# Kernel tuning notes

Hardware: AMD Instinct MI355X
Metric: run time of the kernel (lower is better)

Reference implementation:

```python
import jax, jax.numpy as jnp
import numpy as np

D_MODEL = 768
NUM_HEADS = 12
HEAD_DIM = D_MODEL // NUM_HEADS
SEQ = 4096
BATCH = 1


def setup_inputs() -> dict:
    key = jax.random.key(0)
    ks = jax.random.split(key, 6)
    scale = 1.0 / np.sqrt(D_MODEL)
    x = jax.random.normal(ks[0], (BATCH, SEQ, D_MODEL), dtype=jnp.float32)
    mask = jnp.tril(jnp.ones((SEQ, SEQ), dtype=bool))[None, None]  # [1,1,S,S] causal
    Wq = jax.random.normal(ks[1], (D_MODEL, D_MODEL), dtype=jnp.float32) * scale
    Wk = jax.random.normal(ks[2], (D_MODEL, D_MODEL), dtype=jnp.float32) * scale
    Wv = jax.random.normal(ks[3], (D_MODEL, D_MODEL), dtype=jnp.float32) * scale
    Wo = jax.random.normal(ks[4], (D_MODEL, D_MODEL), dtype=jnp.float32) * scale
    bo = jax.random.normal(ks[5], (D_MODEL,), dtype=jnp.float32) * 0.01
    return {"x": x, "mask": mask, "Wq": Wq, "Wk": Wk, "Wv": Wv, "Wo": Wo, "bo": bo}


def _rope_tables(seq_len, head_dim, dtype):
    # inv_freq over even dims; emb = cat(freqs, freqs) but only the first half
    # participates in the well-defined rotation (x1/x2 have head_dim//2 channels)
    inv_freq = 1.0 / (10000.0 ** (jnp.arange(0, head_dim, 2, dtype=dtype) / head_dim))
    t = jnp.arange(seq_len, dtype=dtype)
    freqs = t[:, None] * inv_freq[None, :]  # [S, head_dim//2]
    return jnp.cos(freqs), jnp.sin(freqs)


def _apply_rotary(xh, cos, sin):
    # xh: [B,H,S,hd]; cos/sin: [S, hd//2]
    x1 = xh[..., ::2]
    x2 = xh[..., 1::2]
    # faithful to source: concatenated (not interleaved) rotated halves
    return jnp.concatenate([x1 * cos - x2 * sin, x1 * sin + x2 * cos], axis=-1)


def reference(x, mask, Wq, Wk, Wv, Wo, bo):
    B, S, D = x.shape
    H, hd = NUM_HEADS, HEAD_DIM
    def split_heads(y):
        return y.reshape(B, S, H, hd).transpose(0, 2, 1, 3)  # [B,H,S,hd]
    q = split_heads(x @ Wq.T)
    k = split_heads(x @ Wk.T)
    v = split_heads(x @ Wv.T)
    cos, sin = _rope_tables(S, hd, x.dtype)
    q = _apply_rotary(q, cos, sin)
    k = _apply_rotary(k, cos, sin)
    scores = jnp.einsum('bhqd,bhkd->bhqk', q, k) / jnp.sqrt(jnp.asarray(hd, x.dtype))
    scores = jnp.where(mask, scores, jnp.asarray(-1e9, x.dtype))
    attn = jax.nn.softmax(scores, axis=-1)  # dropout is identity in eval
    out = jnp.einsum('bhqk,bhkd->bhqd', attn, v)
    out = out.transpose(0, 2, 1, 3).reshape(B, S, D)
    return out @ Wo.T + bo
```

## Files before the change

kernel.cpp:

```cpp
#include <hip/hip_runtime.h>
#include <hip/hip_bf16.h>
#include <math.h>

#define SEQ 4096
#define DM  768
#define NH  12
#define HD  64
#define PER ((size_t)NH * SEQ * HD)
#define XN  ((size_t)SEQ * DM)
#define WN  ((size_t)DM * DM)

typedef __attribute__((ext_vector_type(8))) short bf16x8;
typedef __attribute__((ext_vector_type(4))) short s16x4;
typedef __attribute__((ext_vector_type(4))) float f32x4;

#define MFMA(a, b, c) __builtin_amdgcn_mfma_f32_16x16x32_bf16((a), (b), (c), 0, 0, 0)

#if __has_builtin(__builtin_amdgcn_exp2f)
#define EXP2(x) __builtin_amdgcn_exp2f(x)
#else
#define EXP2(x) exp2f(x)
#endif

#define SWZ(row, blk) (((row) << 6) + ((((blk) ^ ((row) & 7))) << 3))

__device__ __forceinline__ unsigned short f2b(float f) {
    unsigned int u = __float_as_uint(f);
    u += 0x7FFFu + ((u >> 16) & 1u);
    return (unsigned short)(u >> 16);
}

__global__ __launch_bounds__(256) void prep_kernel(
    const float* __restrict__ x,  const float* __restrict__ wq,
    const float* __restrict__ wk, const float* __restrict__ wv,
    const float* __restrict__ wo,
    unsigned short* __restrict__ dstbase, float2* __restrict__ rope)
{
    const float* srcs[5] = {x, wq, wk, wv, wo};
    const size_t n4s[5]  = {XN / 4, WN / 4, WN / 4, WN / 4, WN / 4};
    unsigned short* d = dstbase;
    for (int rg = 0; rg < 5; ++rg) {
        const float4* s4 = (const float4*)srcs[rg];
        s16x4* d4 = (s16x4*)d;
        for (size_t i = (size_t)blockIdx.x * 256 + threadIdx.x; i < n4s[rg];
             i += (size_t)gridDim.x * 256) {
            const float4 v = s4[i];
            s16x4 p;
            p.x = (short)f2b(v.x); p.y = (short)f2b(v.y);
            p.z = (short)f2b(v.z); p.w = (short)f2b(v.w);
            d4[i] = p;
        }
        d += n4s[rg] * 4;
    }
    for (int g = blockIdx.x * 256 + threadIdx.x; g < 131072; g += gridDim.x * 256) {
        const int row = g >> 5, fi = g & 31;
        const float invf = expf(-(float)fi * 0.28782313662425576f);
        float sn, cs;
        sincosf((float)row * invf, &sn, &cs);
        rope[row * 32 + fi] = make_float2(cs, sn);
    }
}

__global__ __launch_bounds__(256) void qkv_mfma(
    const float* __restrict__ x,  const unsigned short* __restrict__ xb,
    const float* __restrict__ Wq, const float* __restrict__ Wk, const float* __restrict__ Wv,
    const unsigned short* __restrict__ Wqb, const unsigned short* __restrict__ Wkb,
    const unsigned short* __restrict__ Wvb,
    const float2* __restrict__ rope,
    unsigned short* __restrict__ Qo, unsigned short* __restrict__ Ko,
    unsigned short* __restrict__ Vo, int fast)
{
    __shared__ __align__(16) unsigned short Xs[2][4096];
    __shared__ __align__(16) unsigned short Ws[2][3][4096];
    __shared__ unsigned short VL[64 * 66];

    const int t    = threadIdx.x;
    const int w    = t >> 6;
    const int lane = t & 63;
    const int quad = lane >> 4;
    const int l16  = lane & 15;

    const int gid = blockIdx.y * 64 + blockIdx.x;
    const int Wl  = (gid & 7) * 96 + (gid >> 3);
    const int h   = Wl % 12;
    const int s0  = (Wl / 12) * 64;
    const int n0  = h * 64;

    const unsigned short* Wbs[3] = {Wqb, Wkb, Wvb};
    const float*          Wfs[3] = {Wq, Wk, Wv};

    const int rowb = 32 * (w >> 1);
    const int colb = 32 * (w & 1);

    f32x4 acc[3][2][2];
    #pragma unroll
    for (int rg = 0; rg < 3; ++rg)
        #pragma unroll
        for (int mi = 0; mi < 2; ++mi)
            #pragma unroll
            for (int ni = 0; ni < 2; ++ni) acc[rg][mi][ni] = (f32x4){0,0,0,0};

    const int prow = t >> 3, pblk = t & 7;

    bf16x8 xr0, xr1, wr0[3], wr1[3];
    if (fast) {
        xr0 = *(const bf16x8*)&xb[(size_t)(s0 + prow) * DM + pblk * 8];
        xr1 = *(const bf16x8*)&xb[(size_t)(s0 + prow + 32) * DM + pblk * 8];
        #pragma unroll
        for (int rg = 0; rg < 3; ++rg) {
            wr0[rg] = *(const bf16x8*)&Wbs[rg][(size_t)(n0 + prow) * DM + pblk * 8];
            wr1[rg] = *(const bf16x8*)&Wbs[rg][(size_t)(n0 + prow + 32) * DM + pblk * 8];
        }
        *(bf16x8*)&Xs[0][SWZ(prow, pblk)]      = xr0;
        *(bf16x8*)&Xs[0][SWZ(prow + 32, pblk)] = xr1;
        #pragma unroll
        for (int rg = 0; rg < 3; ++rg) {
            *(bf16x8*)&Ws[0][rg][SWZ(prow, pblk)]      = wr0[rg];
            *(bf16x8*)&Ws[0][rg][SWZ(prow + 32, pblk)] = wr1[rg];
        }
    } else {
        for (int e = t; e < 1024; e += 256) {
            const int row = e >> 4, c4 = e & 15;
            const int off = SWZ(row, c4 >> 1) + (c4 & 1) * 4;
            const float4 xv = *(const float4*)&x[(size_t)(s0 + row) * DM + c4 * 4];
            s16x4 px; px.x = (short)f2b(xv.x); px.y = (short)f2b(xv.y);
            px.z = (short)f2b(xv.z); px.w = (short)f2b(xv.w);
            *(s16x4*)&Xs[0][off] = px;
            #pragma unroll
            for (int rg = 0; rg < 3; ++rg) {
                const float4 wv = *(const float4*)&Wfs[rg][(size_t)(n0 + row) * DM + c4 * 4];
                s16x4 pw; pw.x = (short)f2b(wv.x); pw.y = (short)f2b(wv.y);
                pw.z = (short)f2b(wv.z); pw.w = (short)f2b(wv.w);
                *(s16x4*)&Ws[0][rg][off] = pw;
            }
        }
    }
    __syncthreads();

    for (int kt = 0; kt < 12; ++kt) {
        const unsigned short* Xb = Xs[kt & 1];
        if (fast && kt < 11) {
            const int k0 = (kt + 1) * 64;
            xr0 = *(const bf16x8*)&xb[(size_t)(s0 + prow) * DM + k0 + pblk * 8];
            xr1 = *(const bf16x8*)&xb[(size_t)(s0 + prow + 32) * DM + k0 + pblk * 8];
            #pragma unroll
            for (int rg = 0; rg < 3; ++rg) {
                wr0[rg] = *(const bf16x8*)&Wbs[rg][(size_t)(n0 + prow) * DM + k0 + pblk * 8];
                wr1[rg] = *(const bf16x8*)&Wbs[rg][(size_t)(n0 + prow + 32) * DM + k0 + pblk * 8];
            }
        }
        bf16x8 a[2][2];
        #pragma unroll
        for (int mi = 0; mi < 2; ++mi)
            #pragma unroll
            for (int hh = 0; hh < 2; ++hh)
                a[mi][hh] = *(const bf16x8*)&Xb[SWZ(rowb + 16 * mi + l16, 4 * hh + quad)];
        #pragma unroll
        for (int rg = 0; rg < 3; ++rg) {
            const unsigned short* Wbt = Ws[kt & 1][rg];
            #pragma unroll
            for (int ni = 0; ni < 2; ++ni) {
                const bf16x8 b0 = *(const bf16x8*)&Wbt[SWZ(colb + 16 * ni + l16, quad)];
                const bf16x8 b1 = *(const bf16x8*)&Wbt[SWZ(colb + 16 * ni + l16, 4 + quad)];
                #pragma unroll
                for (int mi = 0; mi < 2; ++mi) {
                    acc[rg][mi][ni] = MFMA(a[mi][0], b0, acc[rg][mi][ni]);
                    acc[rg][mi][ni] = MFMA(a[mi][1], b1, acc[rg][mi][ni]);
                }
            }
        }
        if (kt < 11) {
            const int nb = (kt + 1) & 1;
            if (fast) {
                *(bf16x8*)&Xs[nb][SWZ(prow, pblk)]      = xr0;
                *(bf16x8*)&Xs[nb][SWZ(prow + 32, pblk)] = xr1;
                #pragma unroll
                for (int rg = 0; rg < 3; ++rg) {
                    *(bf16x8*)&Ws[nb][rg][SWZ(prow, pblk)]      = wr0[rg];
                    *(bf16x8*)&Ws[nb][rg][SWZ(prow + 32, pblk)] = wr1[rg];
                }
            } else {
                const int k0 = (kt + 1) * 64;
                for (int e = t; e < 1024; e += 256) {
                    const int row = e >> 4, c4 = e & 15;
                    const int off = SWZ(row, c4 >> 1) + (c4 & 1) * 4;
                    const float4 xv = *(const float4*)&x[(size_t)(s0 + row) * DM + k0 + c4 * 4];
                    s16x4 px; px.x = (short)f2b(xv.x); px.y = (short)f2b(xv.y);
                    px.z = (short)f2b(xv.z); px.w = (short)f2b(xv.w);
                    *(s16x4*)&Xs[nb][off] = px;
                    #pragma unroll
                    for (int rg = 0; rg < 3; ++rg) {
                        const float4 wv = *(const float4*)&Wfs[rg][(size_t)(n0 + row) * DM + k0 + c4 * 4];
                        s16x4 pw; pw.x = (short)f2b(wv.x); pw.y = (short)f2b(wv.y);
                        pw.z = (short)f2b(wv.z); pw.w = (short)f2b(wv.w);
                        *(s16x4*)&Ws[nb][rg][off] = pw;
                    }
                }
            }
        }
        __syncthreads();
    }

    const size_t headoff = (size_t)h * SEQ * HD;
    #pragma unroll
    for (int rg = 0; rg < 2; ++rg) {
        unsigned short* dst = (rg == 0) ? Qo : Ko;
        const float qsc = (rg == 0) ? 0.18033688011112042f : 1.0f;
        #pragma unroll
        for (int mi = 0; mi < 2; ++mi)
            #pragma unroll
            for (int ni = 0; ni < 2; ++ni)
                #pragma unroll
                for (int r = 0; r < 4; ++r) {
                    const int srow = s0 + rowb + 16 * mi + quad * 4 + r;
                    const int d  = colb + 16 * ni + l16;
                    const int fi = d >> 1;
                    const float own = acc[rg][mi][ni][r] * qsc;
                    const float oth = __shfl_xor(own, 1);
                    float cs, sn;
                    if (fast) {
                        const float2 t2 = rope[srow * 32 + fi];
                        cs = t2.x; sn = t2.y;
                    } else {
                        const float invf = expf(-(float)fi * 0.28782313662425576f);
                        sincosf((float)srow * invf, &sn, &cs);
                    }
                    const float val = (d & 1) ? (oth * sn + own * cs)
                                              : (own * cs - oth * sn);
                    dst[headoff + (size_t)srow * HD + ((d & 1) ? 32 : 0) + fi] = f2b(val);
                }
    }
    #pragma unroll
    for (int mi = 0; mi < 2; ++mi)
        #pragma unroll
        for (int ni = 0; ni < 2; ++ni)
            #pragma unroll
            for (int r = 0; r < 4; ++r)
                VL[(colb + 16 * ni + l16) * 66 + rowb + 16 * mi + quad * 4 + r] =
                    f2b(acc[2][mi][ni][r]);
    __syncthreads();
    for (int e = t; e < 2048; e += 256) {
        const int d = e >> 5, sp = e & 31;
        const unsigned int v = (unsigned int)VL[d * 66 + 2 * sp] |
                               ((unsigned int)VL[d * 66 + 2 * sp + 1] << 16);
        *(unsigned int*)&Vo[headoff + (size_t)d * SEQ + s0 + 2 * sp] = v;
    }
}

__global__ __launch_bounds__(256, 2) void attn_mfma(
    const unsigned short* __restrict__ Q,
    const unsigned short* __restrict__ K,
    const unsigned short* __restrict__ V,
    unsigned short* __restrict__ O,
    float* __restrict__ Part)
{
    __shared__ __align__(16) unsigned char SM[53248];
    unsigned short* Kst = (unsigned short*)SM;
    unsigned short* Vt  = (unsigned short*)(SM + 16384);
    unsigned short* Ps  = (unsigned short*)(SM + 32768);
    float* ACC  = (float*)SM;
    float* ACC2 = (float*)(SM + 32768);
    float* Lx   = (float*)(SM + 51200);

    int h, xx;
    if (gridDim.x == 96) {
        const int gid = blockIdx.y * 96 + blockIdx.x;
        const int Wl  = (gid & 7) * 144 + (gid >> 3);
        h  = Wl / 96;
        xx = Wl - h * 96;
    } else {
        const int gid = blockIdx.y * 64 + blockIdx.x;
        const int Wl  = (gid & 7) * 96 + (gid >> 3);
        h  = Wl >> 6;
        xx = Wl & 63;
    }

    int i, kstart, nch, domask, partial, pslice;
    if (gridDim.x == 96) {
        if (xx < 64) {
            i = 63 - xx; kstart = 0;
            const int full = ((i * 64 + 63) >> 7) + 1;
            nch = full < 16 ? full : 16;
            domask  = (i <= 31);
            partial = (i >= 32); pslice = 0;
        } else {
            i = 127 - xx; kstart = 2048;
            nch = ((i * 64 + 63 - 2048) >> 7) + 1;
            domask = 1; partial = 1; pslice = 1;
        }
    } else {
        i = 63 - xx; kstart = 0;
        nch = ((i * 64 + 63) >> 7) + 1;
        domask = 1; partial = 0; pslice = 0;
    }
    const int q0 = i * 64;

    const int t    = threadIdx.x;
    const int w    = t >> 6;
    const int lane = t & 63;
    const int quad = lane >> 4;
    const int l16  = lane & 15;
    const size_t headoff = (size_t)h * SEQ * HD;

    for (int e = t; e < 512; e += 256) {
        const int row = e >> 3, bp = e & 7, blk = bp ^ (row & 7);
        *(bf16x8*)&Kst[row * 64 + bp * 8] =
            *(const bf16x8*)&Q[headoff + (size_t)(q0 + row) * HD + blk * 8];
    }
    __syncthreads();
    bf16x8 aQ[4][2];
    #pragma unroll
    for (int qt = 0; qt < 4; ++qt)
        #pragma unroll
        for (int hh = 0; hh < 2; ++hh)
            aQ[qt][hh] = *(const bf16x8*)&Kst[SWZ(16 * qt + l16, 4 * hh + quad)];
    __syncthreads();

    bf16x8 kreg[4], vreg[4];
    #pragma unroll
    for (int ii = 0; ii < 4; ++ii) {
        const int e = t + ii * 256, row = e >> 3, bp = e & 7, blk = bp ^ (row & 7);
        kreg[ii] = *(const bf16x8*)&K[headoff + (size_t)(kstart + row) * HD + blk * 8];
    }
    #pragma unroll
    for (int ii = 0; ii < 4; ++ii) {
        const int e = t + ii * 256, row = e >> 4, bp = e & 15, blk = bp ^ (row & 15);
        vreg[ii] = *(const bf16x8*)&V[headoff + (size_t)row * SEQ + kstart + blk * 8];
    }
    #pragma unroll
    for (int ii = 0; ii < 4; ++ii) {
        const int e = t + ii * 256, row = e >> 3, bp = e & 7;
        *(bf16x8*)&Kst[row * 64 + bp * 8] = kreg[ii];
    }
    #pragma unroll
    for (int ii = 0; ii < 4; ++ii) {
        const int e = t + ii * 256, row = e >> 4, bp = e & 15;
        *(bf16x8*)&Vt[row * 128 + bp * 8] = vreg[ii];
    }
    __syncthreads();

    bf16x8 ones;
    #pragma unroll
    for (int ii = 0; ii < 8; ++ii) ones[ii] = (short)0x3F80;

    f32x4 oT[4][4];
    #pragma unroll
    for (int dt = 0; dt < 4; ++dt)
        #pragma unroll
        for (int qt = 0; qt < 4; ++qt) oT[dt][qt] = (f32x4){0,0,0,0};
    f32x4 lT[4] = {{0,0,0,0},{0,0,0,0},{0,0,0,0},{0,0,0,0}};

    unsigned short* usp = Ps + w * 2560;

    for (int c = 0; c < nch; ++c) {
        const int k0 = kstart + c * 128;
        const int last = (c == nch - 1);

        bf16x8 bK[2][2];
        #pragma unroll
        for (int kt = 0; kt < 2; ++kt)
            #pragma unroll
            for (int hh = 0; hh < 2; ++hh)
                bK[kt][hh] = *(const bf16x8*)
                    &Kst[SWZ(32 * w + 16 * kt + l16, 4 * hh + quad)];
        bf16x8 aV[4];
        #pragma unroll
        for (int dt = 0; dt < 4; ++dt) {
            const int row = 16 * dt + l16;
            aV[dt] = *(const bf16x8*)&Vt[row * 128 + (((4 * w + quad) ^ (row & 15)) << 3)];
        }

        if (c + 1 < nch) {
            const int kn = k0 + 128;
            #pragma unroll
            for (int ii = 0; ii < 4; ++ii) {
                const int e = t + ii * 256, row = e >> 3, bp = e & 7, blk = bp ^ (row & 7);
                kreg[ii] = *(const bf16x8*)&K[headoff + (size_t)(kn + row) * HD + blk * 8];
            }
            #pragma unroll
            for (int ii = 0; ii < 4; ++ii) {
                const int e = t + ii * 256, row = e >> 4, bp = e & 15, blk = bp ^ (row & 15);
                vreg[ii] = *(const bf16x8*)&V[headoff + (size_t)row * SEQ + kn + blk * 8];
            }
        }

        #pragma unroll
        for (int qt = 0; qt < 4; ++qt) {
            f32x4 s0 = (f32x4){0,0,0,0}, s1 = (f32x4){0,0,0,0};
            #pragma unroll
            for (int hh = 0; hh < 2; ++hh) {
                s0 = MFMA(aQ[qt][hh], bK[0][hh], s0);
                s1 = MFMA(aQ[qt][hh], bK[1][hh], s1);
            }
            if (domask && last) {
                const int key0 = k0 + 32 * w + l16;
                #pragma unroll
                for (int r = 0; r < 4; ++r) {
                    const int qrow = q0 + 16 * qt + 4 * quad + r;
                    if (key0 > qrow)      s0[r] = -1e30f;
                    if (key0 + 16 > qrow) s1[r] = -1e30f;
                }
            }
            #pragma unroll
            for (int r = 0; r < 4; ++r) {
                const int row = (16 * qt + 4 * quad + r) * 40;
                usp[row + l16]      = f2b(EXP2(s0[r]));
                usp[row + 16 + l16] = f2b(EXP2(s1[r]));
            }
        }

        asm volatile("s_waitcnt lgkmcnt(0)" ::: "memory");

        __builtin_amdgcn_s_setprio(1);
        #pragma unroll
        for (int qt = 0; qt < 4; ++qt) {
            const bf16x8 bP = *(const bf16x8*)&usp[(16 * qt + l16) * 40 + quad * 8];
            lT[qt] = MFMA(ones, bP, lT[qt]);
            #pragma unroll
            for (int dt = 0; dt < 4; ++dt)
                oT[dt][qt] = MFMA(aV[dt], bP, oT[dt][qt]);
        }
        __builtin_amdgcn_s_setprio(0);

        __syncthreads();
        if (c + 1 < nch) {
            #pragma unroll
            for (int ii = 0; ii < 4; ++ii) {
                const int e = t + ii * 256, row = e >> 3, bp = e & 7;
                *(bf16x8*)&Kst[row * 64 + bp * 8] = kreg[ii];
            }
            #pragma unroll
            for (int ii = 0; ii < 4; ++ii) {
                const int e = t + ii * 256, row = e >> 4, bp = e & 15;
                *(bf16x8*)&Vt[row * 128 + bp * 8] = vreg[ii];
            }
        }
        __syncthreads();
    }

    if (w != 0 && quad == 0) {
        #pragma unroll
        for (int qt = 0; qt < 4; ++qt)
            Lx[w * 64 + 16 * qt + l16] = lT[qt][0];
    }
    if (w == 1) {
        #pragma unroll
        for (int dt = 0; dt < 4; ++dt)
            #pragma unroll
            for (int qt = 0; qt < 4; ++qt)
                *(f32x4*)&ACC[(16 * qt + l16) * 72 + 16 * dt + 4 * quad] = oT[dt][qt];
    }
    __syncthreads();
    if (w == 0) {
        #pragma unroll
        for (int dt = 0; dt < 4; ++dt)
            #pragma unroll
            for (int qt = 0; qt < 4; ++qt)
                oT[dt][qt] += *(const f32x4*)&ACC[(16 * qt + l16) * 72 + 16 * dt + 4 * quad];
    }
    if (w == 2) {
        #pragma unroll
        for (int dt = 0; dt < 4; ++dt)
            #pragma unroll
            for (int qt = 0; qt < 4; ++qt)
                *(f32x4*)&ACC2[(16 * qt + l16) * 72 + 16 * dt + 4 * quad] = oT[dt][qt];
    }
    __syncthreads();
    if (w == 0) {
        #pragma unroll
        for (int dt = 0; dt < 4; ++dt)
            #pragma unroll
            for (int qt = 0; qt < 4; ++qt)
                oT[dt][qt] += *(const f32x4*)&ACC2[(16 * qt + l16) * 72 + 16 * dt + 4 * quad];
    }
    if (w == 3) {
        #pragma unroll
        for (int dt = 0; dt < 4; ++dt)
            #pragma unroll
            for (int qt = 0; qt < 4; ++qt)
                *(f32x4*)&ACC[(16 * qt + l16) * 72 + 16 * dt + 4 * quad] = oT[dt][qt];
    }
    __syncthreads();
    if (w == 0) {
        float ls[4];
        #pragma unroll
        for (int qt = 0; qt < 4; ++qt) {
            #pragma unroll
            for (int dt = 0; dt < 4; ++dt)
                oT[dt][qt] += *(const f32x4*)&ACC[(16 * qt + l16) * 72 + 16 * dt + 4 * quad];
            ls[qt] = lT[qt][0] + Lx[64 + 16 * qt + l16] +
                     Lx[128 + 16 * qt + l16] + Lx[192 + 16 * qt + l16];
        }
        if (!partial) {
            #pragma unroll
            for (int qt = 0; qt < 4; ++qt) {
                const float inv = 1.0f / ls[qt];
                const size_t rowoff = (size_t)(q0 + 16 * qt + l16) * DM + h * HD;
                #pragma unroll
                for (int dt = 0; dt < 4; ++dt) {
                    ushort4 u;
                    u.x = f2b(oT[dt][qt][0] * inv);
                    u.y = f2b(oT[dt][qt][1] * inv);
                    u.z = f2b(oT[dt][qt][2] * inv);
                    u.w = f2b(oT[dt][qt][3] * inv);
                    *(ushort4*)&O[rowoff + 16 * dt + 4 * quad] = u;
                }
            }
        } else {
            float* P = Part + (size_t)(((i - 32) * 12 + h) * 2 + pslice) * 4160;
            #pragma unroll
            for (int dt = 0; dt < 4; ++dt)
                #pragma unroll
                for (int qt = 0; qt < 4; ++qt)
                    *(f32x4*)&P[(16 * qt + l16) * 64 + 16 * dt + 4 * quad] = oT[dt][qt];
            if (quad == 0) {
                #pragma unroll
                for (int qt = 0; qt < 4; ++qt)
                    P[4096 + 16 * qt + l16] = ls[qt];
            }
        }
    }
}

__global__ __launch_bounds__(256) void reduce_attn(
    const float* __restrict__ Part, unsigned short* __restrict__ O)
{
    const int b  = blockIdx.x;
    const int i  = 32 + b / 12, h = b % 12;
    const int q0 = i * 64;
    const float* P0 = Part + (size_t)(b * 2 + 0) * 4160;
    const float* P1 = Part + (size_t)(b * 2 + 1) * 4160;
    __shared__ float linv[64];
    const int t = threadIdx.x;
    if (t < 64) linv[t] = 1.0f / (P0[4096 + t] + P1[4096 + t]);
    __syncthreads();
    for (int idx = t; idx < 4096; idx += 256) {
        const int q = idx >> 6, d = idx & 63;
        const float v = (P0[q * 64 + d] + P1[q * 64 + d]) * linv[q];
        O[(size_t)(q0 + q) * DM + h * HD + d] = f2b(v);
    }
}

__global__ __launch_bounds__(256) void proj_mfma(
    const unsigned short* __restrict__ A,
    const float* __restrict__ Wo, const unsigned short* __restrict__ Wob,
    const float* __restrict__ bo,
    float* __restrict__ out, int fast)
{
    __shared__ __align__(16) unsigned short Xs[2][4096];
    __shared__ __align__(16) unsigned short Ws[2][4096];

    const int t    = threadIdx.x;
    const int w    = t >> 6;
    const int lane = t & 63;
    const int quad = lane >> 4;
    const int l16  = lane & 15;

    const int gid = blockIdx.y * 64 + blockIdx.x;
    const int Wl  = (gid & 7) * 96 + (gid >> 3);
    const int s0  = (Wl / 12) * 64;
    const int n0  = (Wl % 12) * 64;

    const int prow = t >> 3, pblk = t & 7;

    f32x4 acc[4] = {{0,0,0,0},{0,0,0,0},{0,0,0,0},{0,0,0,0}};

    bf16x8 ar0, ar1, wr0, wr1;
    ar0 = *(const bf16x8*)&A[(size_t)(s0 + prow) * DM + pblk * 8];
    ar1 = *(const bf16x8*)&A[(size_t)(s0 + prow + 32) * DM + pblk * 8];
    *(bf16x8*)&Xs[0][SWZ(prow, pblk)]      = ar0;
    *(bf16x8*)&Xs[0][SWZ(prow + 32, pblk)] = ar1;
    if (fast) {
        wr0 = *(const bf16x8*)&Wob[(size_t)(n0 + prow) * DM + pblk * 8];
        wr1 = *(const bf16x8*)&Wob[(size_t)(n0 + prow + 32) * DM + pblk * 8];
        *(bf16x8*)&Ws[0][SWZ(prow, pblk)]      = wr0;
        *(bf16x8*)&Ws[0][SWZ(prow + 32, pblk)] = wr1;
    } else {
        for (int e = t; e < 1024; e += 256) {
            const int row = e >> 4, c4 = e & 15;
            const float4 wv = *(const float4*)&Wo[(size_t)(n0 + row) * DM + c4 * 4];
            s16x4 pw; pw.x = (short)f2b(wv.x); pw.y = (short)f2b(wv.y);
            pw.z = (short)f2b(wv.z); pw.w = (short)f2b(wv.w);
            *(s16x4*)&Ws[0][SWZ(row, c4 >> 1) + (c4 & 1) * 4] = pw;
        }
    }
    __syncthreads();

    for (int kt = 0; kt < 12; ++kt) {
        const unsigned short* Xb  = Xs[kt & 1];
        const unsigned short* Wbt = Ws[kt & 1];
        if (kt < 11) {
            const int k0 = (kt + 1) * 64;
            ar0 = *(const bf16x8*)&A[(size_t)(s0 + prow) * DM + k0 + pblk * 8];
            ar1 = *(const bf16x8*)&A[(size_t)(s0 + prow + 32) * DM + k0 + pblk * 8];
            if (fast) {
                wr0 = *(const bf16x8*)&Wob[(size_t)(n0 + prow) * DM + k0 + pblk * 8];
                wr1 = *(const bf16x8*)&Wob[(size_t)(n0 + prow + 32) * DM + k0 + pblk * 8];
            }
        }
        const bf16x8 a0 = *(const bf16x8*)&Xb[SWZ(16 * w + l16, quad)];
        const bf16x8 a1 = *(const bf16x8*)&Xb[SWZ(16 * w + l16, 4 + quad)];
        #pragma unroll
        for (int nt = 0; nt < 4; ++nt) {
            const bf16x8 b0 = *(const bf16x8*)&Wbt[SWZ(16 * nt + l16, quad)];
            const bf16x8 b1 = *(const bf16x8*)&Wbt[SWZ(16 * nt + l16, 4 + quad)];
            acc[nt] = MFMA(a0, b0, acc[nt]);
            acc[nt] = MFMA(a1, b1, acc[nt]);
        }
        if (kt < 11) {
            const int nb = (kt + 1) & 1;
            *(bf16x8*)&Xs[nb][SWZ(prow, pblk)]      = ar0;
            *(bf16x8*)&Xs[nb][SWZ(prow + 32, pblk)] = ar1;
            if (fast) {
                *(bf16x8*)&Ws[nb][SWZ(prow, pblk)]      = wr0;
                *(bf16x8*)&Ws[nb][SWZ(prow + 32, pblk)] = wr1;
            } else {
                const int k0 = (kt + 1) * 64;
                for (int e = t; e < 1024; e += 256) {
                    const int row = e >> 4, c4 = e & 15;
                    const float4 wv = *(const float4*)&Wo[(size_t)(n0 + row) * DM + k0 + c4 * 4];
                    s16x4 pw; pw.x = (short)f2b(wv.x); pw.y = (short)f2b(wv.y);
                    pw.z = (short)f2b(wv.z); pw.w = (short)f2b(wv.w);
                    *(s16x4*)&Ws[nb][SWZ(row, c4 >> 1) + (c4 & 1) * 4] = pw;
                }
            }
        }
        __syncthreads();
    }

    #pragma unroll
    for (int nt = 0; nt < 4; ++nt)
        #pragma unroll
        for (int r = 0; r < 4; ++r) {
            const int srow = s0 + 16 * w + quad * 4 + r;
            const int n    = n0 + nt * 16 + l16;
            out[(size_t)srow * DM + n] = acc[nt][r] + bo[n];
        }
}

extern "C" void kernel_launch(void* const* d_in, const int* in_sizes, int n_in,
                              void* d_out, int out_size, void* d_ws, size_t ws_size,
                              hipStream_t stream) {
    const float* x  = (const float*)d_in[0];
    const float* Wq = (const float*)d_in[2];
    const float* Wk = (const float*)d_in[3];
    const float* Wv = (const float*)d_in[4];
    const float* Wo = (const float*)d_in[5];
    const float* bo = (const float*)d_in[6];
    float* out = (float*)d_out;

    unsigned short* U  = (unsigned short*)d_ws;
    unsigned short* Qw = U;
    unsigned short* Kw = U + PER;
    unsigned short* Vw = U + 2 * PER;
    unsigned short* Ow = U + 3 * PER;
    unsigned short* xb  = U + 4 * PER;
    unsigned short* Wqb = xb + XN;
    unsigned short* Wkb = Wqb + WN;
    unsigned short* Wvb = Wkb + WN;
    unsigned short* Wob = Wvb + WN;
    float2* rope = (float2*)(Wob + WN);
    float*  part = (float*)(rope + 4096 * 32);
    const size_t need  = (char*)part - (char*)d_ws;
    const size_t need2 = need + (size_t)384 * 2 * 4160 * 4;
    const int fast  = (ws_size >= need)  ? 1 : 0;
    const int split = (ws_size >= need2) ? 1 : 0;

    if (fast)
        prep_kernel<<<1024, 256, 0, stream>>>(x, Wq, Wk, Wv, Wo, xb, rope);
    qkv_mfma<<<dim3(64, 12), 256, 0, stream>>>(
        x, xb, Wq, Wk, Wv, Wqb, Wkb, Wvb, rope, Qw, Kw, Vw, fast);
    if (split) {
        attn_mfma<<<dim3(96, NH), 256, 0, stream>>>(Qw, Kw, Vw, Ow, part);
        reduce_attn<<<dim3(384), 256, 0, stream>>>(part, Ow);
    } else {
        attn_mfma<<<dim3(64, NH), 256, 0, stream>>>(Qw, Kw, Vw, Ow, part);
    }
    proj_mfma<<<dim3(SEQ / 64, DM / 64), 256, 0, stream>>>(Ow, Wo, Wob, bo, out, fast);
}
```

Baseline: 232.9 us.

## Split causal attention KV range into up to four 1024-key slices per query tile

Replaces the two-way KV split for the upper half of query tiles with a split-K scheme that cuts each query tile's causal key range into 1024-key slices (1 to 4 slices depending on position). The grid grows from 1152 to 1920 blocks, which balances work across CUs and shortens the longest block. The reduce kernel now sums a variable number of partials for tiles 16..63. In exchange there are more partial-result writes and reads, extra workspace, and more redundant Q loads.

```diff
diff --git a/kernel.cpp b/kernel.cpp
--- a/kernel.cpp
+++ b/kernel.cpp
@@ -262,36 +262,31 @@
     float* ACC2 = (float*)(SM + 32768);
     float* Lx   = (float*)(SM + 51200);
 
-    int h, xx;
-    if (gridDim.x == 96) {
-        const int gid = blockIdx.y * 96 + blockIdx.x;
-        const int Wl  = (gid & 7) * 144 + (gid >> 3);
-        h  = Wl / 96;
-        xx = Wl - h * 96;
+    int h, i, kstart, nch, domask, partial, sidx;
+    if (gridDim.x == 1920) {
+        const int gid = blockIdx.x;
+        const int Wl  = (gid & 7) * 240 + (gid >> 3);
+        h = Wl / 160;
+        const int r = Wl % 160;
+        if (r < 64)       { i = 63 - (r >> 2); sidx = r & 3; }
+        else if (r < 112) { const int q = r - 64; const int d3 = q / 3;
+                            i = 47 - d3; sidx = q - 3 * d3; }
+        else if (r < 144) { const int q = r - 112; i = 31 - (q >> 1); sidx = q & 1; }
+        else              { i = 15 - (r - 144); sidx = 0; }
+        const int nsl  = (i >> 4) + 1;
+        kstart = sidx << 10;
+        const int kend = (sidx == nsl - 1) ? (i + 1) * 64 : ((sidx + 1) << 10);
+        nch     = (kend - kstart + 127) >> 7;
+        domask  = (sidx == nsl - 1);
+        partial = (nsl > 1);
     } else {
         const int gid = blockIdx.y * 64 + blockIdx.x;
         const int Wl  = (gid & 7) * 96 + (gid >> 3);
-        h  = Wl >> 6;
-        xx = Wl & 63;
-    }
-
-    int i, kstart, nch, domask, partial, pslice;
-    if (gridDim.x == 96) {
-        if (xx < 64) {
-            i = 63 - xx; kstart = 0;
-            const int full = ((i * 64 + 63) >> 7) + 1;
-            nch = full < 16 ? full : 16;
-            domask  = (i <= 31);
-            partial = (i >= 32); pslice = 0;
-        } else {
-            i = 127 - xx; kstart = 2048;
-            nch = ((i * 64 + 63 - 2048) >> 7) + 1;
-            domask = 1; partial = 1; pslice = 1;
-        }
-    } else {
+        h = Wl >> 6;
+        const int xx = Wl & 63;
         i = 63 - xx; kstart = 0;
         nch = ((i * 64 + 63) >> 7) + 1;
-        domask = 1; partial = 0; pslice = 0;
+        domask = 1; partial = 0; sidx = 0;
     }
     const int q0 = i * 64;
 
@@ -507,7 +502,7 @@
                 }
             }
         } else {
-            float* P = Part + (size_t)(((i - 32) * 12 + h) * 2 + pslice) * 4160;
+            float* P = Part + (size_t)((i * 12 + h) * 4 + sidx) * 4160;
             #pragma unroll
             for (int dt = 0; dt < 4; ++dt)
                 #pragma unroll
@@ -525,19 +520,24 @@
 __global__ __launch_bounds__(256) void reduce_attn(
     const float* __restrict__ Part, unsigned short* __restrict__ O)
 {
-    const int b  = blockIdx.x;
-    const int i  = 32 + b / 12, h = b % 12;
-    const int q0 = i * 64;
-    const float* P0 = Part + (size_t)(b * 2 + 0) * 4160;
-    const float* P1 = Part + (size_t)(b * 2 + 1) * 4160;
+    const int b   = blockIdx.x;
+    const int i   = 16 + b / 12, h = b % 12;
+    const int q0  = i * 64;
+    const int nsl = (i >> 4) + 1;
+    const float* P0 = Part + (size_t)((i * 12 + h) * 4) * 4160;
     __shared__ float linv[64];
     const int t = threadIdx.x;
-    if (t < 64) linv[t] = 1.0f / (P0[4096 + t] + P1[4096 + t]);
+    if (t < 64) {
+        float sum = 0.f;
+        for (int s = 0; s < nsl; ++s) sum += P0[(size_t)s * 4160 + 4096 + t];
+        linv[t] = 1.0f / sum;
+    }
     __syncthreads();
     for (int idx = t; idx < 4096; idx += 256) {
         const int q = idx >> 6, d = idx & 63;
-        const float v = (P0[q * 64 + d] + P1[q * 64 + d]) * linv[q];
-        O[(size_t)(q0 + q) * DM + h * HD + d] = f2b(v);
+        float v = 0.f;
+        for (int s = 0; s < nsl; ++s) v += P0[(size_t)s * 4160 + idx];
+        O[(size_t)(q0 + q) * DM + h * HD + d] = f2b(v * linv[q]);
     }
 }
 
@@ -662,7 +662,7 @@
     float2* rope = (float2*)(Wob + WN);
     float*  part = (float*)(rope + 4096 * 32);
     const size_t need  = (char*)part - (char*)d_ws;
-    const size_t need2 = need + (size_t)384 * 2 * 4160 * 4;
+    const size_t need2 = need + (size_t)3072 * 4160 * 4;
     const int fast  = (ws_size >= need)  ? 1 : 0;
     const int split = (ws_size >= need2) ? 1 : 0;
 
@@ -671,10 +671,10 @@
     qkv_mfma<<<dim3(64, 12), 256, 0, stream>>>(
         x, xb, Wq, Wk, Wv, Wqb, Wkb, Wvb, rope, Qw, Kw, Vw, fast);
     if (split) {
-        attn_mfma<<<dim3(96, NH), 256, 0, stream>>>(Qw, Kw, Vw, Ow, part);
-        reduce_attn<<<dim3(384), 256, 0, stream>>>(part, Ow);
+        attn_mfma<<<dim3(1920, 1), 256, 0, stream>>>(Qw, Kw, Vw, Ow, part);
+        reduce_attn<<<dim3(576), 256, 0, stream>>>(part, Ow);
     } else {
-        attn_mfma<<<dim3(64, NH), 256, 0, stream>>>(Qw, Kw, Vw, Ow, part);
+        attn_mfma<<<dim3(64, 12), 256, 0, stream>>>(Qw, Kw, Vw, Ow, part);
     }
     proj_mfma<<<dim3(SEQ / 64, DM / 64), 256, 0, stream>>>(Ow, Wo, Wob, bo, out, fast);
 }
```

New measurement: 253.1 us. +8.6%, slower.

## Load K and V MFMA fragments directly from global memory, dropping LDS staging

Applied to the files above, without the earlier changes.

The attention kernel no longer stages K and V chunks through shared memory with two block-wide barriers per chunk. Each wave loads its own K and V MFMA operand fragments straight from global memory into registers, prefetching the next K chunk during the PV phase. This cuts LDS traffic and synchronization and shrinks shared memory, which may allow more resident blocks. The cost is global loads with less coalescing, partly strided V reads across SEQ, and V loads that are no longer prefetched, so their latency may be exposed.

```diff
diff --git a/kernel.cpp b/kernel.cpp
--- a/kernel.cpp
+++ b/kernel.cpp
@@ -254,13 +254,12 @@
     unsigned short* __restrict__ O,
     float* __restrict__ Part)
 {
-    __shared__ __align__(16) unsigned char SM[53248];
-    unsigned short* Kst = (unsigned short*)SM;
-    unsigned short* Vt  = (unsigned short*)(SM + 16384);
-    unsigned short* Ps  = (unsigned short*)(SM + 32768);
+    __shared__ __align__(16) unsigned char SM[39936];
+    unsigned short* Ps  = (unsigned short*)SM;
+    unsigned short* Qst = (unsigned short*)(SM + 20480);
     float* ACC  = (float*)SM;
-    float* ACC2 = (float*)(SM + 32768);
-    float* Lx   = (float*)(SM + 51200);
+    float* ACC2 = (float*)(SM + 20480);
+    float* Lx   = (float*)(SM + 38912);
 
     int h, xx;
     if (gridDim.x == 96) {
@@ -301,10 +300,12 @@
     const int quad = lane >> 4;
     const int l16  = lane & 15;
     const size_t headoff = (size_t)h * SEQ * HD;
+    const unsigned short* Kg = K + headoff;
+    const unsigned short* Vg = V + headoff;
 
     for (int e = t; e < 512; e += 256) {
         const int row = e >> 3, bp = e & 7, blk = bp ^ (row & 7);
-        *(bf16x8*)&Kst[row * 64 + bp * 8] =
+        *(bf16x8*)&Qst[row * 64 + bp * 8] =
             *(const bf16x8*)&Q[headoff + (size_t)(q0 + row) * HD + blk * 8];
     }
     __syncthreads();
@@ -313,31 +314,16 @@
     for (int qt = 0; qt < 4; ++qt)
         #pragma unroll
         for (int hh = 0; hh < 2; ++hh)
-            aQ[qt][hh] = *(const bf16x8*)&Kst[SWZ(16 * qt + l16, 4 * hh + quad)];
-    __syncthreads();
-
-    bf16x8 kreg[4], vreg[4];
-    #pragma unroll
-    for (int ii = 0; ii < 4; ++ii) {
-        const int e = t + ii * 256, row = e >> 3, bp = e & 7, blk = bp ^ (row & 7);
-        kreg[ii] = *(const bf16x8*)&K[headoff + (size_t)(kstart + row) * HD + blk * 8];
-    }
-    #pragma unroll
-    for (int ii = 0; ii < 4; ++ii) {
-        const int e = t + ii * 256, row = e >> 4, bp = e & 15, blk = bp ^ (row & 15);
-        vreg[ii] = *(const bf16x8*)&V[headoff + (size_t)row * SEQ + kstart + blk * 8];
-    }
-    #pragma unroll
-    for (int ii = 0; ii < 4; ++ii) {
-        const int e = t + ii * 256, row = e >> 3, bp = e & 7;
-        *(bf16x8*)&Kst[row * 64 + bp * 8] = kreg[ii];
-    }
-    #pragma unroll
-    for (int ii = 0; ii < 4; ++ii) {
-        const int e = t + ii * 256, row = e >> 4, bp = e & 15;
-        *(bf16x8*)&Vt[row * 128 + bp * 8] = vreg[ii];
-    }
-    __syncthreads();
+            aQ[qt][hh] = *(const bf16x8*)&Qst[SWZ(16 * qt + l16, 4 * hh + quad)];
+
+    bf16x8 kf00, kf01, kf10, kf11;
+    {
+        const size_t kr = (size_t)(kstart + 32 * w + l16) * HD + quad * 8;
+        kf00 = *(const bf16x8*)&Kg[kr];
+        kf01 = *(const bf16x8*)&Kg[kr + 32];
+        kf10 = *(const bf16x8*)&Kg[kr + 16 * HD];
+        kf11 = *(const bf16x8*)&Kg[kr + 16 * HD + 32];
+    }
 
     bf16x8 ones;
     #pragma unroll
@@ -356,42 +342,19 @@
         const int k0 = kstart + c * 128;
         const int last = (c == nch - 1);
 
-        bf16x8 bK[2][2];
-        #pragma unroll
-        for (int kt = 0; kt < 2; ++kt)
-            #pragma unroll
-            for (int hh = 0; hh < 2; ++hh)
-                bK[kt][hh] = *(const bf16x8*)
-                    &Kst[SWZ(32 * w + 16 * kt + l16, 4 * hh + quad)];
-        bf16x8 aV[4];
-        #pragma unroll
-        for (int dt = 0; dt < 4; ++dt) {
-            const int row = 16 * dt + l16;
-            aV[dt] = *(const bf16x8*)&Vt[row * 128 + (((4 * w + quad) ^ (row & 15)) << 3)];
-        }
-
-        if (c + 1 < nch) {
-            const int kn = k0 + 128;
-            #pragma unroll
-            for (int ii = 0; ii < 4; ++ii) {
-                const int e = t + ii * 256, row = e >> 3, bp = e & 7, blk = bp ^ (row & 7);
-                kreg[ii] = *(const bf16x8*)&K[headoff + (size_t)(kn + row) * HD + blk * 8];
-            }
-            #pragma unroll
-            for (int ii = 0; ii < 4; ++ii) {
-                const int e = t + ii * 256, row = e >> 4, bp = e & 15, blk = bp ^ (row & 15);
-                vreg[ii] = *(const bf16x8*)&V[headoff + (size_t)row * SEQ + kn + blk * 8];
-            }
-        }
+        const size_t vr = (size_t)l16 * SEQ + k0 + 32 * w + quad * 8;
+        const bf16x8 vf0 = *(const bf16x8*)&Vg[vr];
+        const bf16x8 vf1 = *(const bf16x8*)&Vg[vr + 16 * SEQ];
+        const bf16x8 vf2 = *(const bf16x8*)&Vg[vr + 32 * SEQ];
+        const bf16x8 vf3 = *(const bf16x8*)&Vg[vr + 48 * SEQ];
 
         #pragma unroll
         for (int qt = 0; qt < 4; ++qt) {
             f32x4 s0 = (f32x4){0,0,0,0}, s1 = (f32x4){0,0,0,0};
-            #pragma unroll
-            for (int hh = 0; hh < 2; ++hh) {
-                s0 = MFMA(aQ[qt][hh], bK[0][hh], s0);
-                s1 = MFMA(aQ[qt][hh], bK[1][hh], s1);
-            }
+            s0 = MFMA(aQ[qt][0], kf00, s0);
+            s0 = MFMA(aQ[qt][1], kf01, s0);
+            s1 = MFMA(aQ[qt][0], kf10, s1);
+            s1 = MFMA(aQ[qt][1], kf11, s1);
             if (domask && last) {
                 const int key0 = k0 + 32 * w + l16;
                 #pragma unroll
@@ -409,6 +372,14 @@
             }
         }
 
+        if (c + 1 < nch) {
+            const size_t kr = (size_t)(k0 + 128 + 32 * w + l16) * HD + quad * 8;
+            kf00 = *(const bf16x8*)&Kg[kr];
+            kf01 = *(const bf16x8*)&Kg[kr + 32];
+            kf10 = *(const bf16x8*)&Kg[kr + 16 * HD];
+            kf11 = *(const bf16x8*)&Kg[kr + 16 * HD + 32];
+        }
+
         asm volatile("s_waitcnt lgkmcnt(0)" ::: "memory");
 
         __builtin_amdgcn_s_setprio(1);
@@ -416,28 +387,15 @@
         for (int qt = 0; qt < 4; ++qt) {
             const bf16x8 bP = *(const bf16x8*)&usp[(16 * qt + l16) * 40 + quad * 8];
             lT[qt] = MFMA(ones, bP, lT[qt]);
-            #pragma unroll
-            for (int dt = 0; dt < 4; ++dt)
-                oT[dt][qt] = MFMA(aV[dt], bP, oT[dt][qt]);
+            oT[0][qt] = MFMA(vf0, bP, oT[0][qt]);
+            oT[1][qt] = MFMA(vf1, bP, oT[1][qt]);
+            oT[2][qt] = MFMA(vf2, bP, oT[2][qt]);
+            oT[3][qt] = MFMA(vf3, bP, oT[3][qt]);
         }
         __builtin_amdgcn_s_setprio(0);
-
-        __syncthreads();
-        if (c + 1 < nch) {
-            #pragma unroll
-            for (int ii = 0; ii < 4; ++ii) {
-                const int e = t + ii * 256, row = e >> 3, bp = e & 7;
-                *(bf16x8*)&Kst[row * 64 + bp * 8] = kreg[ii];
-            }
-            #pragma unroll
-            for (int ii = 0; ii < 4; ++ii) {
-                const int e = t + ii * 256, row = e >> 4, bp = e & 15;
-                *(bf16x8*)&Vt[row * 128 + bp * 8] = vreg[ii];
-            }
-        }
-        __syncthreads();
-    }
-
+    }
+
+    __syncthreads();
     if (w != 0 && quad == 0) {
         #pragma unroll
         for (int qt = 0; qt < 4; ++qt)
@@ -674,7 +632,7 @@
         attn_mfma<<<dim3(96, NH), 256, 0, stream>>>(Qw, Kw, Vw, Ow, part);
         reduce_attn<<<dim3(384), 256, 0, stream>>>(part, Ow);
     } else {
-        attn_mfma<<<dim3(64, NH), 256, 0, stream>>>(Qw, Kw, Vw, Ow, part);
+        attn_mfma<<<dim3(64, 12), 256, 0, stream>>>(Qw, Kw, Vw, Ow, part);
     }
     proj_mfma<<<dim3(SEQ / 64, DM / 64), 256, 0, stream>>>(Ow, Wo, Wob, bo, out, fast);
 }
```

Result: no change. 233.5 us (+0.2%).
